# Kernel tuning notes

Hardware: AMD Instinct MI355X
Metric: run time of the kernel (lower is better)

## Reference

```python
import jax, jax.numpy as jnp
import numpy as np

T, B = 128, 256      # seq_len, batch
D = 1024             # input_dim (embedding dim)
H = 1024             # hidden_dim
NQ = 8               # n_qubits
V = 32000            # vocab_size
TAGS = 1024          # tagset_size


def setup_inputs() -> dict:
    key = jax.random.key(0)
    ks = jax.random.split(key, 10)
    s = 0.05
    return {
        "sentence": jax.random.randint(ks[0], (T, B), 0, V),
        "emb": jax.random.normal(ks[1], (V, D), jnp.float32) * s,
        # gate order: forget, input, update, output (stacked on leading axis)
        "Wg": jax.random.normal(ks[2], (4, D + H, NQ), jnp.float32) * s,
        "bg": jax.random.normal(ks[3], (4, NQ), jnp.float32) * s,
        "theta": jax.random.normal(ks[4], (4, NQ), jnp.float32) * s,  # trainable RX angles
        "Wp": jax.random.normal(ks[5], (4, NQ, H), jnp.float32) * s,
        "bp": jax.random.normal(ks[6], (4, H), jnp.float32) * s,
        "W_tag": jax.random.normal(ks[7], (H, TAGS), jnp.float32) * s,
        "b_tag": jax.random.normal(ks[8], (TAGS,), jnp.float32) * s,
    }


def reference(sentence, emb, Wg, bg, theta, Wp, bp, W_tag, b_tag):
    embeds = emb[sentence]                      # (T, B, D)
    bsz = embeds.shape[1]
    hidden = Wp.shape[2]

    def step(carry, x):
        hx, cx = carry
        comb = jnp.concatenate([x, hx], axis=1)                       # (B, D+H)
        raw = jnp.einsum('bc,gcq->gbq', comb, Wg) + bg[:, None, :]    # (4, B, NQ)
        # QLayer: RX(x) then trainable RX(theta) per wire on |0>, measure Z
        # -> product state, <Z_i> = cos(raw_i + theta_i)  (exact)
        q = jnp.cos(raw + theta[:, None, :])                          # (4, B, NQ)
        proj = jnp.einsum('gbq,gqh->gbh', q, Wp) + bp[:, None, :]     # (4, B, H)
        f = jax.nn.sigmoid(proj[0])
        i = jax.nn.sigmoid(proj[1])
        g = jnp.tanh(proj[2])
        o = jax.nn.sigmoid(proj[3])
        cx = f * cx + i * g
        hx = o * jnp.tanh(cx)
        return (hx, cx), hx

    hx0 = jnp.zeros((bsz, hidden), embeds.dtype)
    cx0 = jnp.zeros((bsz, hidden), embeds.dtype)
    _, lstm_out = jax.lax.scan(step, (hx0, cx0), embeds)              # (T, B, H)
    tag_logits = lstm_out @ W_tag + b_tag                             # (T, B, TAGS)
    # torch applies log_softmax over dim=1 (the batch axis) -- faithful
    return jax.nn.log_softmax(tag_logits, axis=1)
```

## Files before the change

kernel.cpp:

```cpp
#include <hip/hip_runtime.h>
#include <hip/hip_bf16.h>
#include <stdint.h>

#define T_LEN 128
#define B_SZ  256
#define D_IN  1024
#define H_DIM 1024
#define NQ    8
#define VOCAB 32000
#define TAGS  1024

typedef __attribute__((ext_vector_type(8))) short short8;
typedef __attribute__((ext_vector_type(4))) float f32x4;

__device__ __forceinline__ unsigned short f2bf_bits(float x) {
    __hip_bfloat16 h = __float2bfloat16(x);
    unsigned short u; __builtin_memcpy(&u, &h, 2); return u;
}
__device__ __forceinline__ uint32_t pack_bf2(float a, float b) {
    return (uint32_t)f2bf_bits(a) | ((uint32_t)f2bf_bits(b) << 16);
}
__device__ __forceinline__ float sigmoid_f(float x) {
    return 1.f / (1.f + __expf(-x));
}
__device__ __forceinline__ float tanh_f(float x) {
    return 1.f - 2.f / (__expf(2.f * x) + 1.f);
}
__device__ __forceinline__ void gload_lds16(void* lds_base, const void* gptr) {
    __builtin_amdgcn_global_load_lds(
        (__attribute__((address_space(1))) const void*)gptr,
        (__attribute__((address_space(3))) void*)lds_base,
        16, 0, 0);
}

__global__ __launch_bounds__(256) void k_wt_transpose(const float* __restrict__ W,
                                                      __hip_bfloat16* __restrict__ WtT) {
    __shared__ float tile[32][33];
    const int kb = blockIdx.x * 32, nb = blockIdx.y * 32;
    const int r = threadIdx.x >> 5, c = threadIdx.x & 31;
#pragma unroll
    for (int i = 0; i < 4; ++i)
        tile[r + 8 * i][c] = W[(size_t)(kb + r + 8 * i) * TAGS + nb + c];
    __syncthreads();
#pragma unroll
    for (int i = 0; i < 4; ++i)
        WtT[(size_t)(nb + r + 8 * i) * H_DIM + kb + c] = __float2bfloat16(tile[c][r + 8 * i]);
}

#define GXB_ROWS 32
__global__ __launch_bounds__(256, 2) void k_gx(
    const int* __restrict__ sent, const float* __restrict__ emb,
    const float* __restrict__ Wg, const float* __restrict__ bg,
    const float* __restrict__ theta, float* __restrict__ gx)
{
    __shared__ float xs[2][1024];
    const int tid = threadIdx.x, lane = tid & 63, wv = tid >> 6;
    const int ol = lane & 7, s = lane >> 3;
    const int o = wv * 8 + ol;

    float wk[128];
#pragma unroll
    for (int k = 0; k < 32; ++k)
#pragma unroll
        for (int e = 0; e < 4; ++e) {
            const int c = (s + 8 * k) * 4 + e;
            wk[4 * k + e] = Wg[((size_t)wv * 2048 + c) * 8 + ol];
        }
    const float bt = bg[o] + theta[o];

    const int rbase = blockIdx.x * GXB_ROWS;
    const float4* emb4 = (const float4*)emb;
    float4 xn = emb4[(size_t)sent[rbase] * 256 + tid];
    *(float4*)&xs[0][4 * tid] = xn;
    __syncthreads();

    float aPrev = 0.f; int rPrev = -1;
    int cur = 0;
    for (int i = 0; i < GXB_ROWS; ++i) {
        if (i + 1 < GXB_ROWS)
            xn = emb4[(size_t)sent[rbase + i + 1] * 256 + tid];
        if (rPrev >= 0 && lane < 8)
            gx[(size_t)rPrev * 32 + wv * 8 + lane] = aPrev;

        const float4* x4 = (const float4*)xs[cur];
        float a0 = 0.f, a1 = 0.f, a2 = 0.f, a3 = 0.f;
#pragma unroll
        for (int k = 0; k < 32; ++k) {
            float4 v = x4[s + 8 * k];
            a0 = fmaf(wk[4 * k + 0], v.x, a0);
            a1 = fmaf(wk[4 * k + 1], v.y, a1);
            a2 = fmaf(wk[4 * k + 2], v.z, a2);
            a3 = fmaf(wk[4 * k + 3], v.w, a3);
        }
        float a = (a0 + a1) + (a2 + a3);
#pragma unroll
        for (int d = 8; d < 64; d <<= 1) a += __shfl_xor(a, d, 64);
        aPrev = a + bt; rPrev = rbase + i;

        if (i + 1 < GXB_ROWS)
            *(float4*)&xs[cur ^ 1][4 * tid] = xn;
        __syncthreads();
        cur ^= 1;
    }
    if (lane < 8) gx[(size_t)rPrev * 32 + wv * 8 + lane] = aPrev;
}

__global__ __launch_bounds__(512, 2) void k_qlstm(
    const float* __restrict__ gx, const float* __restrict__ Wg,
    const float* __restrict__ Wp, const float* __restrict__ bp,
    __hip_bfloat16* __restrict__ hb)
{
    __shared__ float hs[1024];
    __shared__ __attribute__((aligned(16))) float qs[32];
    __shared__ float gxl[T_LEN * 32];

    const int tid = threadIdx.x, lane = tid & 63, wv = tid >> 6;
    const int b = blockIdx.x;
    const int ol = lane & 3, s = lane >> 2;
    const int o = 4 * wv + ol;
    const int g = o >> 3, q = o & 7;

    float wg[64];
#pragma unroll
    for (int k = 0; k < 16; ++k)
#pragma unroll
        for (int e = 0; e < 4; ++e) {
            const int c = (s + 16 * k) * 4 + e;
            wg[4 * k + e] = Wg[((size_t)g * 2048 + 1024 + c) * 8 + q];
        }
    float wpA[32], wpB[32];
#pragma unroll
    for (int j = 0; j < 32; ++j) {
        wpA[j] = Wp[(size_t)j * H_DIM + 2 * tid];
        wpB[j] = Wp[(size_t)j * H_DIM + 2 * tid + 1];
    }
    float bpA[4], bpB[4];
#pragma unroll
    for (int gg = 0; gg < 4; ++gg) {
        bpA[gg] = bp[gg * H_DIM + 2 * tid];
        bpB[gg] = bp[gg * H_DIM + 2 * tid + 1];
    }

#pragma unroll
    for (int i = tid; i < T_LEN * 32; i += 512)
        gxl[i] = gx[((size_t)(i >> 5) * B_SZ + b) * 32 + (i & 31)];

    *(float2*)&hs[2 * tid] = (float2){0.f, 0.f};
    float cx0 = 0.f, cx1 = 0.f;
    uint32_t hvp = 0;
    __syncthreads();

    uint32_t* hb32 = (uint32_t*)hb;
    for (int t = 0; t < T_LEN; ++t) {
        if (t > 0)
            hb32[((size_t)(t - 1) * B_SZ + b) * 512 + tid] = hvp;

        const float4* h4 = (const float4*)hs;
        float a0 = 0.f, a1 = 0.f, a2 = 0.f, a3 = 0.f;
#pragma unroll
        for (int k = 0; k < 16; ++k) {
            float4 v = h4[s + 16 * k];
            a0 = fmaf(wg[4 * k + 0], v.x, a0);
            a1 = fmaf(wg[4 * k + 1], v.y, a1);
            a2 = fmaf(wg[4 * k + 2], v.z, a2);
            a3 = fmaf(wg[4 * k + 3], v.w, a3);
        }
        float a = (a0 + a1) + (a2 + a3);
#pragma unroll
        for (int d = 4; d < 64; d <<= 1) a += __shfl_xor(a, d, 64);
        if (lane < 4)
            qs[4 * wv + lane] = __cosf(a + gxl[t * 32 + 4 * wv + lane]);
        __syncthreads();

        const float4* q4 = (const float4*)qs;
        float pjA[4], pjB[4];
#pragma unroll
        for (int gg = 0; gg < 4; ++gg) {
            float4 u = q4[2 * gg], v = q4[2 * gg + 1];
            pjA[gg] = bpA[gg]
                    + u.x * wpA[gg * 8 + 0] + u.y * wpA[gg * 8 + 1]
                    + u.z * wpA[gg * 8 + 2] + u.w * wpA[gg * 8 + 3]
                    + v.x * wpA[gg * 8 + 4] + v.y * wpA[gg * 8 + 5]
                    + v.z * wpA[gg * 8 + 6] + v.w * wpA[gg * 8 + 7];
            pjB[gg] = bpB[gg]
                    + u.x * wpB[gg * 8 + 0] + u.y * wpB[gg * 8 + 1]
                    + u.z * wpB[gg * 8 + 2] + u.w * wpB[gg * 8 + 3]
                    + v.x * wpB[gg * 8 + 4] + v.y * wpB[gg * 8 + 5]
                    + v.z * wpB[gg * 8 + 6] + v.w * wpB[gg * 8 + 7];
        }
        const float fA = sigmoid_f(pjA[0]), iA = sigmoid_f(pjA[1]);
        const float gA = tanh_f(pjA[2]),   oA = sigmoid_f(pjA[3]);
        const float fB = sigmoid_f(pjB[0]), iB = sigmoid_f(pjB[1]);
        const float gB = tanh_f(pjB[2]),   oB = sigmoid_f(pjB[3]);
        cx0 = fA * cx0 + iA * gA;
        cx1 = fB * cx1 + iB * gB;
        const float hv0 = oA * tanh_f(cx0);
        const float hv1 = oB * tanh_f(cx1);
        *(float2*)&hs[2 * tid] = (float2){hv0, hv1};
        hvp = pack_bf2(hv0, hv1);
        __syncthreads();
    }
    hb32[((size_t)(T_LEN - 1) * B_SZ + b) * 512 + tid] = hvp;
}

__global__ __launch_bounds__(256) void k_tag_gemm(const __hip_bfloat16* __restrict__ Hb,
                                                  const __hip_bfloat16* __restrict__ WtT,
                                                  float* __restrict__ out)
{
    __shared__ short As[128 * 32];
    __shared__ short Bs[128 * 32];
    const int m0 = blockIdx.x * 128, n0 = blockIdx.y * 128;
    const int tid = threadIdx.x, lane = tid & 63, wid = tid >> 6;
    const int wm = (wid & 1) * 64, wn = (wid >> 1) * 64;
    const int mrow = lane & 15, quad = lane >> 4;

    const short* Hs = (const short*)Hb;
    const short* Ws = (const short*)WtT;

    f32x4 acc[4][4];
#pragma unroll
    for (int mi = 0; mi < 4; ++mi)
#pragma unroll
        for (int ni = 0; ni < 4; ++ni)
            acc[mi][ni] = (f32x4){0.f, 0.f, 0.f, 0.f};

    for (int kt = 0; kt < 32; ++kt) {
        const int k0 = kt * 32;
        __syncthreads();
#pragma unroll
        for (int ch = 0; ch < 2; ++ch) {
            const int chunk = wid + ch * 4;
            const int row = chunk * 16 + (lane >> 2);
            const int kc = (lane & 3) * 8;
            gload_lds16(&As[chunk * 512], &Hs[(size_t)(m0 + row) * H_DIM + k0 + kc]);
            gload_lds16(&Bs[chunk * 512], &Ws[(size_t)(n0 + row) * H_DIM + k0 + kc]);
        }
        __syncthreads();

        short8 afr[4], bfr[4];
#pragma unroll
        for (int mi = 0; mi < 4; ++mi)
            afr[mi] = *(const short8*)&As[(wm + mi * 16 + mrow) * 32 + quad * 8];
#pragma unroll
        for (int ni = 0; ni < 4; ++ni)
            bfr[ni] = *(const short8*)&Bs[(wn + ni * 16 + mrow) * 32 + quad * 8];
#pragma unroll
        for (int mi = 0; mi < 4; ++mi)
#pragma unroll
            for (int ni = 0; ni < 4; ++ni)
                acc[mi][ni] = __builtin_amdgcn_mfma_f32_16x16x32_bf16(
                    afr[mi], bfr[ni], acc[mi][ni], 0, 0, 0);
    }

#pragma unroll
    for (int mi = 0; mi < 4; ++mi)
#pragma unroll
        for (int ni = 0; ni < 4; ++ni)
#pragma unroll
            for (int r = 0; r < 4; ++r) {
                const int grow = m0 + wm + mi * 16 + quad * 4 + r;
                const int gcol = n0 + wn + ni * 16 + mrow;
                out[(size_t)grow * TAGS + gcol] = acc[mi][ni][r];
            }
}

__global__ __launch_bounds__(256) void k_logsoftmax(float* __restrict__ out) {
    const int t = blockIdx.x;
    const int n = blockIdx.y * 256 + threadIdx.x;
    float* base = out + (size_t)t * B_SZ * TAGS + n;
    float m = -1e30f;
    for (int b = 0; b < B_SZ; ++b) m = fmaxf(m, base[(size_t)b * TAGS]);
    float s = 0.f;
    for (int b = 0; b < B_SZ; ++b) s += __expf(base[(size_t)b * TAGS] - m);
    const float lse = m + __logf(s);
    for (int b = 0; b < B_SZ; ++b) base[(size_t)b * TAGS] -= lse;
}

extern "C" void kernel_launch(void* const* d_in, const int* in_sizes, int n_in,
                              void* d_out, int out_size, void* d_ws, size_t ws_size,
                              hipStream_t stream) {
    (void)in_sizes; (void)n_in; (void)out_size; (void)ws_size;
    const int*   sent  = (const int*)d_in[0];
    const float* emb   = (const float*)d_in[1];
    const float* Wg    = (const float*)d_in[2];
    const float* bg    = (const float*)d_in[3];
    const float* theta = (const float*)d_in[4];
    const float* Wp    = (const float*)d_in[5];
    const float* bp    = (const float*)d_in[6];
    const float* Wt    = (const float*)d_in[7];
    float* out = (float*)d_out;

    __hip_bfloat16* hb  = (__hip_bfloat16*)d_ws;
    __hip_bfloat16* WtT = (__hip_bfloat16*)((char*)d_ws + (size_t)64 * 1024 * 1024);
    float* gx = (float*)d_out;

    k_wt_transpose<<<dim3(32, 32), 256, 0, stream>>>(Wt, WtT);
    k_gx<<<dim3((T_LEN * B_SZ) / GXB_ROWS), 256, 0, stream>>>(sent, emb, Wg, bg, theta, gx);
    k_qlstm<<<dim3(B_SZ), 512, 0, stream>>>(gx, Wg, Wp, bp, hb);
    k_tag_gemm<<<dim3(256, 8), 256, 0, stream>>>(hb, WtT, out);
    k_logsoftmax<<<dim3(T_LEN, 4), 256, 0, stream>>>(out);
}
```

Baseline: 691.2 us.

## Use MFMA for recurrent gate matvec, batch stores, tile logsoftmax through LDS

The recurrent h·Wg product in the LSTM kernel moves from per-lane FP32 FMAs over an fp32 h buffer to bf16 MFMA with a bf16 h buffer in shared memory. Partial sums are reduced across waves through LDS, which adds one more barrier per step. The gx and hidden-state global stores are now buffered over 8 steps and written in groups. The log-softmax kernel is restructured to stage a 256x32 tile in LDS and use more blocks, replacing strided global passes. Computing h in bf16 adds precision risk.

```diff
diff --git a/kernel.cpp b/kernel.cpp
--- a/kernel.cpp
+++ b/kernel.cpp
@@ -74,35 +74,42 @@
     *(float4*)&xs[0][4 * tid] = xn;
     __syncthreads();
 
-    float aPrev = 0.f; int rPrev = -1;
     int cur = 0;
-    for (int i = 0; i < GXB_ROWS; ++i) {
-        if (i + 1 < GXB_ROWS)
-            xn = emb4[(size_t)sent[rbase + i + 1] * 256 + tid];
-        if (rPrev >= 0 && lane < 8)
-            gx[(size_t)rPrev * 32 + wv * 8 + lane] = aPrev;
-
-        const float4* x4 = (const float4*)xs[cur];
-        float a0 = 0.f, a1 = 0.f, a2 = 0.f, a3 = 0.f;
-#pragma unroll
-        for (int k = 0; k < 32; ++k) {
-            float4 v = x4[s + 8 * k];
-            a0 = fmaf(wk[4 * k + 0], v.x, a0);
-            a1 = fmaf(wk[4 * k + 1], v.y, a1);
-            a2 = fmaf(wk[4 * k + 2], v.z, a2);
-            a3 = fmaf(wk[4 * k + 3], v.w, a3);
-        }
-        float a = (a0 + a1) + (a2 + a3);
-#pragma unroll
-        for (int d = 8; d < 64; d <<= 1) a += __shfl_xor(a, d, 64);
-        aPrev = a + bt; rPrev = rbase + i;
-
-        if (i + 1 < GXB_ROWS)
-            *(float4*)&xs[cur ^ 1][4 * tid] = xn;
-        __syncthreads();
-        cur ^= 1;
-    }
-    if (lane < 8) gx[(size_t)rPrev * 32 + wv * 8 + lane] = aPrev;
+    for (int i8 = 0; i8 < GXB_ROWS / 8; ++i8) {
+        float gacc[8];
+#pragma unroll
+        for (int ii = 0; ii < 8; ++ii) {
+            const int i = i8 * 8 + ii;
+            const bool havenext = (i + 1 < GXB_ROWS);
+            if (havenext)
+                xn = emb4[(size_t)sent[rbase + i + 1] * 256 + tid];
+
+            const float4* x4 = (const float4*)xs[cur];
+            float a0 = 0.f, a1 = 0.f, a2 = 0.f, a3 = 0.f;
+#pragma unroll
+            for (int k = 0; k < 32; ++k) {
+                float4 v = x4[s + 8 * k];
+                a0 = fmaf(wk[4 * k + 0], v.x, a0);
+                a1 = fmaf(wk[4 * k + 1], v.y, a1);
+                a2 = fmaf(wk[4 * k + 2], v.z, a2);
+                a3 = fmaf(wk[4 * k + 3], v.w, a3);
+            }
+            float a = (a0 + a1) + (a2 + a3);
+#pragma unroll
+            for (int d = 8; d < 64; d <<= 1) a += __shfl_xor(a, d, 64);
+            gacc[ii] = a + bt;
+
+            if (havenext)
+                *(float4*)&xs[cur ^ 1][4 * tid] = xn;
+            __syncthreads();
+            cur ^= 1;
+        }
+        if (lane < 8) {
+#pragma unroll
+            for (int ii = 0; ii < 8; ++ii)
+                gx[(size_t)(rbase + i8 * 8 + ii) * 32 + wv * 8 + lane] = gacc[ii];
+        }
+    }
 }
 
 __global__ __launch_bounds__(512, 2) void k_qlstm(
@@ -110,24 +117,32 @@
     const float* __restrict__ Wp, const float* __restrict__ bp,
     __hip_bfloat16* __restrict__ hb)
 {
-    __shared__ float hs[1024];
+    __shared__ uint32_t hsb[512];
+    __shared__ float red[8 * 32];
     __shared__ __attribute__((aligned(16))) float qs[32];
     __shared__ float gxl[T_LEN * 32];
 
     const int tid = threadIdx.x, lane = tid & 63, wv = tid >> 6;
     const int b = blockIdx.x;
-    const int ol = lane & 3, s = lane >> 2;
-    const int o = 4 * wv + ol;
-    const int g = o >> 3, q = o & 7;
-
-    float wg[64];
-#pragma unroll
-    for (int k = 0; k < 16; ++k)
-#pragma unroll
-        for (int e = 0; e < 4; ++e) {
-            const int c = (s + 16 * k) * 4 + e;
-            wg[4 * k + e] = Wg[((size_t)g * 2048 + 1024 + c) * 8 + q];
-        }
+    const int lg = lane >> 4;
+    const int K0 = wv * 128;
+
+    union { short8 s8; uint32_t u[4]; } wf[2][4];
+#pragma unroll
+    for (int ro = 0; ro < 2; ++ro) {
+        const int o = ro * 16 + (lane & 15);
+        const int g = o >> 3, q = o & 7;
+#pragma unroll
+        for (int kt = 0; kt < 4; ++kt) {
+            const int k0 = K0 + kt * 32 + lg * 8;
+#pragma unroll
+            for (int p = 0; p < 4; ++p) {
+                float e0 = Wg[((size_t)g * 2048 + 1024 + k0 + 2 * p) * 8 + q];
+                float e1 = Wg[((size_t)g * 2048 + 1024 + k0 + 2 * p + 1) * 8 + q];
+                wf[ro][kt].u[p] = pack_bf2(e0, e1);
+            }
+        }
+    }
     float wpA[32], wpB[32];
 #pragma unroll
     for (int j = 0; j < 32; ++j) {
@@ -141,66 +156,76 @@
         bpB[gg] = bp[gg * H_DIM + 2 * tid + 1];
     }
 
-#pragma unroll
     for (int i = tid; i < T_LEN * 32; i += 512)
         gxl[i] = gx[((size_t)(i >> 5) * B_SZ + b) * 32 + (i & 31)];
 
-    *(float2*)&hs[2 * tid] = (float2){0.f, 0.f};
+    hsb[tid] = 0u;
     float cx0 = 0.f, cx1 = 0.f;
-    uint32_t hvp = 0;
     __syncthreads();
 
     uint32_t* hb32 = (uint32_t*)hb;
-    for (int t = 0; t < T_LEN; ++t) {
-        if (t > 0)
-            hb32[((size_t)(t - 1) * B_SZ + b) * 512 + tid] = hvp;
-
-        const float4* h4 = (const float4*)hs;
-        float a0 = 0.f, a1 = 0.f, a2 = 0.f, a3 = 0.f;
-#pragma unroll
-        for (int k = 0; k < 16; ++k) {
-            float4 v = h4[s + 16 * k];
-            a0 = fmaf(wg[4 * k + 0], v.x, a0);
-            a1 = fmaf(wg[4 * k + 1], v.y, a1);
-            a2 = fmaf(wg[4 * k + 2], v.z, a2);
-            a3 = fmaf(wg[4 * k + 3], v.w, a3);
-        }
-        float a = (a0 + a1) + (a2 + a3);
-#pragma unroll
-        for (int d = 4; d < 64; d <<= 1) a += __shfl_xor(a, d, 64);
-        if (lane < 4)
-            qs[4 * wv + lane] = __cosf(a + gxl[t * 32 + 4 * wv + lane]);
-        __syncthreads();
-
-        const float4* q4 = (const float4*)qs;
-        float pjA[4], pjB[4];
-#pragma unroll
-        for (int gg = 0; gg < 4; ++gg) {
-            float4 u = q4[2 * gg], v = q4[2 * gg + 1];
-            pjA[gg] = bpA[gg]
-                    + u.x * wpA[gg * 8 + 0] + u.y * wpA[gg * 8 + 1]
-                    + u.z * wpA[gg * 8 + 2] + u.w * wpA[gg * 8 + 3]
-                    + v.x * wpA[gg * 8 + 4] + v.y * wpA[gg * 8 + 5]
-                    + v.z * wpA[gg * 8 + 6] + v.w * wpA[gg * 8 + 7];
-            pjB[gg] = bpB[gg]
-                    + u.x * wpB[gg * 8 + 0] + u.y * wpB[gg * 8 + 1]
-                    + u.z * wpB[gg * 8 + 2] + u.w * wpB[gg * 8 + 3]
-                    + v.x * wpB[gg * 8 + 4] + v.y * wpB[gg * 8 + 5]
-                    + v.z * wpB[gg * 8 + 6] + v.w * wpB[gg * 8 + 7];
-        }
-        const float fA = sigmoid_f(pjA[0]), iA = sigmoid_f(pjA[1]);
-        const float gA = tanh_f(pjA[2]),   oA = sigmoid_f(pjA[3]);
-        const float fB = sigmoid_f(pjB[0]), iB = sigmoid_f(pjB[1]);
-        const float gB = tanh_f(pjB[2]),   oB = sigmoid_f(pjB[3]);
-        cx0 = fA * cx0 + iA * gA;
-        cx1 = fB * cx1 + iB * gB;
-        const float hv0 = oA * tanh_f(cx0);
-        const float hv1 = oB * tanh_f(cx1);
-        *(float2*)&hs[2 * tid] = (float2){hv0, hv1};
-        hvp = pack_bf2(hv0, hv1);
-        __syncthreads();
-    }
-    hb32[((size_t)(T_LEN - 1) * B_SZ + b) * 512 + tid] = hvp;
+    const f32x4 zf = (f32x4){0.f, 0.f, 0.f, 0.f};
+
+    for (int t8 = 0; t8 < T_LEN / 8; ++t8) {
+        uint32_t hv8[8];
+#pragma unroll
+        for (int tt = 0; tt < 8; ++tt) {
+            const int t = t8 * 8 + tt;
+
+            f32x4 p0 = zf, p1 = zf;
+#pragma unroll
+            for (int kt = 0; kt < 4; ++kt) {
+                short8 bf = *(const short8*)((const char*)hsb + 2 * K0 + 64 * kt + lg * 16);
+                p0 = __builtin_amdgcn_mfma_f32_16x16x32_bf16(wf[0][kt].s8, bf, p0, 0, 0, 0);
+                p1 = __builtin_amdgcn_mfma_f32_16x16x32_bf16(wf[1][kt].s8, bf, p1, 0, 0, 0);
+            }
+            if ((lane & 15) == 0) {
+                *(f32x4*)&red[wv * 32 + 4 * lg] = p0;
+                *(f32x4*)&red[wv * 32 + 16 + 4 * lg] = p1;
+            }
+            __syncthreads();
+
+            if (tid < 32) {
+                float r = gxl[t * 32 + tid];
+#pragma unroll
+                for (int w = 0; w < 8; ++w) r += red[w * 32 + tid];
+                qs[tid] = __cosf(r);
+            }
+            __syncthreads();
+
+            const float4* q4 = (const float4*)qs;
+            float pjA[4], pjB[4];
+#pragma unroll
+            for (int gg = 0; gg < 4; ++gg) {
+                float4 u = q4[2 * gg], v = q4[2 * gg + 1];
+                pjA[gg] = bpA[gg]
+                        + u.x * wpA[gg * 8 + 0] + u.y * wpA[gg * 8 + 1]
+                        + u.z * wpA[gg * 8 + 2] + u.w * wpA[gg * 8 + 3]
+                        + v.x * wpA[gg * 8 + 4] + v.y * wpA[gg * 8 + 5]
+                        + v.z * wpA[gg * 8 + 6] + v.w * wpA[gg * 8 + 7];
+                pjB[gg] = bpB[gg]
+                        + u.x * wpB[gg * 8 + 0] + u.y * wpB[gg * 8 + 1]
+                        + u.z * wpB[gg * 8 + 2] + u.w * wpB[gg * 8 + 3]
+                        + v.x * wpB[gg * 8 + 4] + v.y * wpB[gg * 8 + 5]
+                        + v.z * wpB[gg * 8 + 6] + v.w * wpB[gg * 8 + 7];
+            }
+            const float fA = sigmoid_f(pjA[0]), iA = sigmoid_f(pjA[1]);
+            const float gA = tanh_f(pjA[2]),   oA = sigmoid_f(pjA[3]);
+            const float fB = sigmoid_f(pjB[0]), iB = sigmoid_f(pjB[1]);
+            const float gB = tanh_f(pjB[2]),   oB = sigmoid_f(pjB[3]);
+            cx0 = fA * cx0 + iA * gA;
+            cx1 = fB * cx1 + iB * gB;
+            const float hv0 = oA * tanh_f(cx0);
+            const float hv1 = oB * tanh_f(cx1);
+            const uint32_t hvp = pack_bf2(hv0, hv1);
+            hsb[tid] = hvp;
+            hv8[tt] = hvp;
+            __syncthreads();
+        }
+#pragma unroll
+        for (int tt = 0; tt < 8; ++tt)
+            hb32[((size_t)(t8 * 8 + tt) * B_SZ + b) * 512 + tid] = hv8[tt];
+    }
 }
 
 __global__ __launch_bounds__(256) void k_tag_gemm(const __hip_bfloat16* __restrict__ Hb,
@@ -264,16 +289,31 @@
             }
 }
 
+#define LSM_COLS 32
 __global__ __launch_bounds__(256) void k_logsoftmax(float* __restrict__ out) {
-    const int t = blockIdx.x;
-    const int n = blockIdx.y * 256 + threadIdx.x;
-    float* base = out + (size_t)t * B_SZ * TAGS + n;
-    float m = -1e30f;
-    for (int b = 0; b < B_SZ; ++b) m = fmaxf(m, base[(size_t)b * TAGS]);
-    float s = 0.f;
-    for (int b = 0; b < B_SZ; ++b) s += __expf(base[(size_t)b * TAGS] - m);
-    const float lse = m + __logf(s);
-    for (int b = 0; b < B_SZ; ++b) base[(size_t)b * TAGS] -= lse;
+    __shared__ float tile[256 * LSM_COLS];
+    __shared__ float lse[LSM_COLS];
+    const int t = blockIdx.x, n0 = blockIdx.y * LSM_COLS;
+    const int tid = threadIdx.x;
+    float* base = out + (size_t)t * B_SZ * TAGS + n0;
+
+    for (int i = tid; i < 256 * LSM_COLS; i += 256) {
+        const int b = i >> 5, c = i & (LSM_COLS - 1);
+        tile[i] = base[(size_t)b * TAGS + c];
+    }
+    __syncthreads();
+    if (tid < LSM_COLS) {
+        float m = -1e30f;
+        for (int b = 0; b < 256; ++b) m = fmaxf(m, tile[b * LSM_COLS + tid]);
+        float s = 0.f;
+        for (int b = 0; b < 256; ++b) s += __expf(tile[b * LSM_COLS + tid] - m);
+        lse[tid] = m + __logf(s);
+    }
+    __syncthreads();
+    for (int i = tid; i < 256 * LSM_COLS; i += 256) {
+        const int b = i >> 5, c = i & (LSM_COLS - 1);
+        base[(size_t)b * TAGS + c] = tile[i] - lse[c];
+    }
 }
 
 extern "C" void kernel_launch(void* const* d_in, const int* in_sizes, int n_in,
@@ -298,5 +338,5 @@
     k_gx<<<dim3((T_LEN * B_SZ) / GXB_ROWS), 256, 0, stream>>>(sent, emb, Wg, bg, theta, gx);
     k_qlstm<<<dim3(B_SZ), 512, 0, stream>>>(gx, Wg, Wp, bp, hb);
     k_tag_gemm<<<dim3(256, 8), 256, 0, stream>>>(hb, WtT, out);
-    k_logsoftmax<<<dim3(T_LEN, 4), 256, 0, stream>>>(out);
-}
+    k_logsoftmax<<<dim3(T_LEN, TAGS / LSM_COLS), 256, 0, stream>>>(out);
+}
```

New measurement: 628.3 us. -9.1%, faster.
